# Optimization experiments

Measured on AMD Instinct MI355X. Metric: run time of the kernel, lower is better.

## Reference

```python
import jax, jax.numpy as jnp
import numpy as np

N = 100000      # nodes
E = 500000      # edges
F_IN = 165      # Elliptic feature dim
HID = 128       # hidden
HEADS = 2
DH = HID // HEADS  # 64, per-head GAT out dim
EPS = 1e-5


def setup_inputs() -> dict:
    key = jax.random.key(0)
    ks = jax.random.split(key, 40)

    def w(k, shape, fan_in):
        return (jax.random.normal(k, shape, jnp.float32) / np.sqrt(fan_in)).astype(jnp.float32)

    def bn_params(k, d):
        k1, k2 = jax.random.split(k)
        return (jnp.ones((d,), jnp.float32),                       # gamma
                jnp.zeros((d,), jnp.float32),                      # beta
                0.1 * jax.random.normal(k1, (d,), jnp.float32),    # running mean
                jax.random.uniform(k2, (d,), jnp.float32, 0.5, 1.5))  # running var

    bn1 = bn_params(ks[10], HID)
    bn2 = bn_params(ks[11], HID)
    bn3 = bn_params(ks[12], DH)

    return {
        "x": jax.random.normal(ks[0], (N, F_IN), jnp.float32),
        "edge_index": jax.random.randint(ks[1], (2, E), 0, N, jnp.int32),
        # input_proj
        "w_in": w(ks[2], (F_IN, HID), F_IN), "b_in": jnp.zeros((HID,), jnp.float32),
        # GCNConv
        "w_gcn": w(ks[3], (HID, HID), HID), "b_gcn": jnp.zeros((HID,), jnp.float32),
        "bn1_g": bn1[0], "bn1_b": bn1[1], "bn1_m": bn1[2], "bn1_v": bn1[3],
        # GATConv (heads=2, out=64, concat)
        "w_gat": w(ks[4], (HID, HEADS * DH), HID),
        "att_src": 0.1 * jax.random.normal(ks[5], (HEADS, DH), jnp.float32),
        "att_dst": 0.1 * jax.random.normal(ks[6], (HEADS, DH), jnp.float32),
        "b_gat": jnp.zeros((HEADS * DH,), jnp.float32),
        "bn2_g": bn2[0], "bn2_b": bn2[1], "bn2_m": bn2[2], "bn2_v": bn2[3],
        # SAGEConv (mean aggr)
        "w_sage_l": w(ks[7], (HID, DH), HID), "b_sage": jnp.zeros((DH,), jnp.float32),
        "w_sage_r": w(ks[8], (HID, DH), HID),
        "bn3_g": bn3[0], "bn3_b": bn3[1], "bn3_m": bn3[2], "bn3_v": bn3[3],
        # residual proj + classifier
        "w_res": w(ks[9], (HID, DH), HID), "b_res": jnp.zeros((DH,), jnp.float32),
        "w_c1": w(ks[13], (DH, 32), DH), "b_c1": jnp.zeros((32,), jnp.float32),
        "w_c2": w(ks[14], (32, 2), 32), "b_c2": jnp.zeros((2,), jnp.float32),
    }


def _bn(h, g, b, m, v):
    # eval-mode BatchNorm1d with running stats
    return (h - m) * (g / jnp.sqrt(v + EPS)) + b


def reference(x, edge_index, w_in, b_in, w_gcn, b_gcn,
              bn1_g, bn1_b, bn1_m, bn1_v,
              w_gat, att_src, att_dst, b_gat,
              bn2_g, bn2_b, bn2_m, bn2_v,
              w_sage_l, b_sage, w_sage_r,
              bn3_g, bn3_b, bn3_m, bn3_v,
              w_res, b_res, w_c1, b_c1, w_c2, b_c2):
    n = x.shape[0]
    src, dst = edge_index[0], edge_index[1]
    loop = jnp.arange(n, dtype=src.dtype)
    src_l = jnp.concatenate([src, loop])   # edges + self loops (GCN & GAT)
    dst_l = jnp.concatenate([dst, loop])

    # ---- input_proj (dropout = identity in eval) ----
    h = jax.nn.elu(x @ w_in + b_in)
    residual = h

    hw = h @ w_gcn
    deg = jax.ops.segment_sum(jnp.ones_like(dst_l, jnp.float32), dst_l, n)
    dinv = jnp.where(deg > 0, jax.lax.rsqrt(deg), 0.0)
    norm = dinv[src_l] * dinv[dst_l]                      # [E+N]
    h1 = jax.ops.segment_sum(hw[src_l] * norm[:, None], dst_l, n) + b_gcn
    h1 = jax.nn.elu(_bn(h1, bn1_g, bn1_b, bn1_m, bn1_v))

    # ---- GATConv (heads=2, concat, self loops, leaky_relu 0.2) ----
    g = (h1 @ w_gat).reshape(n, HEADS, DH)
    a_src = jnp.sum(g * att_src, axis=-1)                 # [N, H]
    a_dst = jnp.sum(g * att_dst, axis=-1)
    e = jax.nn.leaky_relu(a_src[src_l] + a_dst[dst_l], 0.2)   # [E+N, H]
    mx = jax.ops.segment_max(e, dst_l, n)                 # per-dst softmax max
    ex = jnp.exp(e - mx[dst_l])
    denom = jax.ops.segment_sum(ex, dst_l, n)
    alpha = ex / (denom[dst_l] + 1e-16)                   # [E+N, H]
    h2 = jax.ops.segment_sum(g[src_l] * alpha[:, :, None], dst_l, n)
    h2 = h2.reshape(n, HEADS * DH) + b_gat
    h2 = jax.nn.elu(_bn(h2, bn2_g, bn2_b, bn2_m, bn2_v))

    # ---- SAGEConv: W_l mean(neighbors) + W_r x + b (no self loops) ----
    deg_s = jax.ops.segment_sum(jnp.ones_like(dst, jnp.float32), dst, n)
    mean_nb = jax.ops.segment_sum(h2[src], dst, n) / jnp.maximum(deg_s, 1.0)[:, None]
    h3 = mean_nb @ w_sage_l + b_sage + h2 @ w_sage_r
    h3 = _bn(h3, bn3_g, bn3_b, bn3_m, bn3_v)
    h3 = jax.nn.elu(h3 + residual @ w_res + b_res)

    # ---- classifier ----
    z = jax.nn.elu(h3 @ w_c1 + b_c1)
    return z @ w_c2 + b_c2
```

## Files before the change

### kernel.cpp

```cpp
#include <hip/hip_runtime.h>
#include <cstdint>
#include <cstddef>

#define BN_EPS 1e-5f

typedef __attribute__((ext_vector_type(8))) short short8v;
typedef __attribute__((ext_vector_type(4))) float float4v;
typedef __attribute__((ext_vector_type(4))) unsigned int uint4v;
typedef unsigned int uint32;
typedef unsigned short ushort16;

__device__ __forceinline__ float elu_f(float v){ return v > 0.f ? v : expm1f(v); }
__device__ __forceinline__ float leaky_f(float v){ return v > 0.f ? v : 0.2f*v; }
__device__ __forceinline__ uint32 f2bf(float f){
  uint32 b = __float_as_uint(f);
  return (b + 0x7fffu + ((b >> 16) & 1u)) >> 16;
}
__device__ __forceinline__ float bflo(uint32 u){ return __uint_as_float(u << 16); }
__device__ __forceinline__ float bfhi(uint32 u){ return __uint_as_float(u & 0xffff0000u); }
__device__ __forceinline__ float readlane_f(float v, int l){
  return __int_as_float(__builtin_amdgcn_readlane(__float_as_int(v), l));
}


__global__ void count_deg_kernel(const int* __restrict__ dst, int E, int* __restrict__ cnt){
  int i = blockIdx.x*blockDim.x + threadIdx.x;
  if(i < E) atomicAdd(&cnt[dst[i]], 1);
}

__global__ __launch_bounds__(1024) void scan_blocks(const int* __restrict__ cnt, int n,
                                                    int* __restrict__ part, int* __restrict__ bsum){
  __shared__ int wsum[16];
  int tid = threadIdx.x, lane = tid & 63, w = tid >> 6;
  int i = blockIdx.x*1024 + tid;
  int v = (i < n) ? cnt[i] : 0;
  int sv = v;
#pragma unroll
  for(int o = 1; o < 64; o <<= 1){
    int u = __shfl_up(sv, o);
    if(lane >= o) sv += u;
  }
  if(lane == 63) wsum[w] = sv;
  __syncthreads();
  int woff = 0;
#pragma unroll
  for(int q = 0; q < 16; q++) woff += (q < w) ? wsum[q] : 0;
  if(i < n) part[i] = woff + sv - v;
  if(tid == 1023) bsum[blockIdx.x] = woff + sv;
}

__global__ __launch_bounds__(1024) void scan_bsum(const int* __restrict__ bsum, int nb,
                                                  int* __restrict__ boff, int* __restrict__ rowptr, int n){
  __shared__ int wsum[16];
  int tid = threadIdx.x, lane = tid & 63, w = tid >> 6;
  int v = (tid < nb) ? bsum[tid] : 0;
  int sv = v;
#pragma unroll
  for(int o = 1; o < 64; o <<= 1){
    int u = __shfl_up(sv, o);
    if(lane >= o) sv += u;
  }
  if(lane == 63) wsum[w] = sv;
  __syncthreads();
  int woff = 0;
#pragma unroll
  for(int q = 0; q < 16; q++) woff += (q < w) ? wsum[q] : 0;
  if(tid < nb) boff[tid] = woff + sv - v;
  if(tid == 1023) rowptr[n] = woff + sv;
}

__global__ void scan_add_dinv(const int* __restrict__ part, const int* __restrict__ boff,
                              const int* __restrict__ cnt, int n,
                              int* __restrict__ rowptr, float* __restrict__ dinv){
  int i = blockIdx.x*blockDim.x + threadIdx.x;
  if(i < n){
    rowptr[i] = part[i] + boff[i >> 10];
    dinv[i] = rsqrtf((float)cnt[i] + 1.0f);
  }
}

__global__ void scatter_kernel(const int* __restrict__ src, const int* __restrict__ dst, int E,
                               const int* __restrict__ rowptr, int* __restrict__ fill,
                               int* __restrict__ col){
  int i = blockIdx.x*blockDim.x + threadIdx.x;
  if(i < E){
    int s = src[i], d = dst[i];
    int p = rowptr[d] + atomicAdd(&fill[d], 1);
    col[p] = s;
  }
}


__global__ __launch_bounds__(256) void cvt_x(const float* __restrict__ x, uint2* __restrict__ xb, int total){
  int idx = blockIdx.x*256 + threadIdx.x;
  if(idx >= total) return;
  int row = idx/48;
  int cp = idx - row*48;
  int c = cp*4;
  const float* xr = x + (size_t)row*165;
  float v0 = (c   < 165) ? xr[c]   : 0.f;
  float v1 = (c+1 < 165) ? xr[c+1] : 0.f;
  float v2 = (c+2 < 165) ? xr[c+2] : 0.f;
  float v3 = (c+3 < 165) ? xr[c+3] : 0.f;
  xb[idx] = make_uint2(f2bf(v0) | (f2bf(v1) << 16), f2bf(v2) | (f2bf(v3) << 16));
}


__global__ void prep_scales(const float* __restrict__ bn1_g, const float* __restrict__ bn1_b,
    const float* __restrict__ bn1_m, const float* __restrict__ bn1_v, const float* __restrict__ b_gcn,
    const float* __restrict__ bn2_g, const float* __restrict__ bn2_b,
    const float* __restrict__ bn2_m, const float* __restrict__ bn2_v, const float* __restrict__ b_gat,
    const float* __restrict__ att_s, const float* __restrict__ att_d,
    const float* __restrict__ bn3_g, const float* __restrict__ bn3_b,
    const float* __restrict__ bn3_m, const float* __restrict__ bn3_v,
    const float* __restrict__ b_sage, const float* __restrict__ b_res,
    float* __restrict__ s1, float* __restrict__ b1c,
    float* __restrict__ s2, float* __restrict__ b2c,
    float* __restrict__ atts2, float* __restrict__ attd2,
    float* __restrict__ s3, float* __restrict__ bias3){
  int c = threadIdx.x;
  float v1 = bn1_g[c]*rsqrtf(bn1_v[c] + BN_EPS);
  s1[c] = v1;
  b1c[c] = (b_gcn[c] - bn1_m[c])*v1 + bn1_b[c];
  float v2 = bn2_g[c]*rsqrtf(bn2_v[c] + BN_EPS);
  s2[c] = v2;
  b2c[c] = (b_gat[c] - bn2_m[c])*v2 + bn2_b[c];
  atts2[c] = att_s[c]/v2;
  attd2[c] = att_d[c]/v2;
  if(c < 64){
    float v3 = bn3_g[c]*rsqrtf(bn3_v[c] + BN_EPS);
    s3[c] = v3;
    bias3[c] = (b_sage[c] - bn3_m[c])*v3 + bn3_b[c] + b_res[c];
  }
}


__device__ __forceinline__ void pack_region(const float* __restrict__ W, int K, int NOUT, int kbase, int idx,
                                            const float* __restrict__ scale, ushort16* __restrict__ out){
  int k = idx / NOUT, c = idx - k*NOUT;
  float v = (k < K) ? W[(size_t)k*NOUT + c] : 0.f;
  if(scale) v *= scale[c];
  int pk = kbase + k;
  out[(size_t)(pk >> 3)*NOUT*8 + (size_t)c*8 + (pk & 7)] = (ushort16)f2bf(v);
}

__global__ __launch_bounds__(256) void pack_all(const float* __restrict__ w_in, const float* __restrict__ w_gcn,
    const float* __restrict__ w_gat, const float* __restrict__ w_sl, const float* __restrict__ w_sr,
    const float* __restrict__ w_res,
    const float* __restrict__ s1, const float* __restrict__ s2, const float* __restrict__ s3,
    ushort16* __restrict__ pw_in, ushort16* __restrict__ pw_gcn,
    ushort16* __restrict__ pw_gat, ushort16* __restrict__ pw_cat){
  int b = blockIdx.x, t = threadIdx.x;
  if(b < 96)       pack_region(w_in,  165, 128, 0,   b*256 + t,        nullptr, pw_in);
  else if(b < 160) pack_region(w_gcn, 128, 128, 0,   (b-96)*256 + t,   s1,      pw_gcn);
  else if(b < 224) pack_region(w_gat, 128, 128, 0,   (b-160)*256 + t,  s2,      pw_gat);
  else if(b < 256) pack_region(w_sl,  128, 64,  0,   (b-224)*256 + t,  s3,      pw_cat);
  else if(b < 288) pack_region(w_sr,  128, 64,  128, (b-256)*256 + t,  s3,      pw_cat);
  else             pack_region(w_res, 128, 64,  256, (b-288)*256 + t,  nullptr, pw_cat);
}


template<int KSTEPS, int NOUT, int EPI>
__global__ __launch_bounds__(256) void mfma_gemm(
    const ushort16* __restrict__ A, int lda,
    const uint4v* __restrict__ pw,
    const float* __restrict__ bias,
    void* __restrict__ out, int ldo, int N,
    const float* __restrict__ dinv,
    const float* __restrict__ atts2, const float* __restrict__ attd2,
    float* __restrict__ a_src, float* __restrict__ a_dst,
    float* __restrict__ ess)
{
  constexpr int SLICE = 4*NOUT;
  constexpr int PT = SLICE/256;
  __shared__ uint4v wlds[2][SLICE];
  int t = threadIdx.x;
  int wid = t >> 6, lane = t & 63;
  int wm, wn;
  if(NOUT == 128){ wm = wid >> 1; wn = wid & 1; } else { wm = wid; wn = 0; }
  constexpr int MTILE = (NOUT == 128) ? 128 : 256;
  long row0 = (long)blockIdx.x*MTILE + wm*64;
  int l15 = lane & 15, lk = lane >> 4;
  int wn64 = wn*64;

  float4v acc[4][4];
#pragma unroll
  for(int fm = 0; fm < 4; fm++)
#pragma unroll
    for(int fn = 0; fn < 4; fn++) acc[fm][fn] = (float4v){0.f,0.f,0.f,0.f};

  const ushort16* abase[4];
#pragma unroll
  for(int fm = 0; fm < 4; fm++){
    long r = row0 + fm*16 + l15;
    if(r > (long)N - 1) r = (long)N - 1;
    abase[fm] = A + r*(size_t)lda + lk*8;
  }

  uint4v rst[PT];
#pragma unroll
  for(int i = 0; i < PT; i++) rst[i] = pw[i*256 + t];
#pragma unroll
  for(int i = 0; i < PT; i++) wlds[0][i*256 + t] = rst[i];
  if(KSTEPS > 1){
#pragma unroll
    for(int i = 0; i < PT; i++) rst[i] = pw[SLICE + i*256 + t];
  }
  short8v a[4];
#pragma unroll
  for(int fm = 0; fm < 4; fm++) a[fm] = *(const short8v*)(abase[fm]);
  __syncthreads();

#pragma unroll
  for(int ks = 0; ks < KSTEPS; ks++){
    short8v b[4];
#pragma unroll
    for(int fn = 0; fn < 4; fn++)
      b[fn] = *(const short8v*)&wlds[ks & 1][lk*NOUT + wn64 + fn*16 + l15];
    short8v an[4];
    if(ks + 1 < KSTEPS){
#pragma unroll
      for(int fm = 0; fm < 4; fm++) an[fm] = *(const short8v*)(abase[fm] + (ks + 1)*32);
    }
#pragma unroll
    for(int fm = 0; fm < 4; fm++)
#pragma unroll
      for(int fn = 0; fn < 4; fn++)
        acc[fm][fn] = __builtin_amdgcn_mfma_f32_16x16x32_bf16(b[fn], a[fm], acc[fm][fn], 0, 0, 0);
    if(ks + 1 < KSTEPS){
#pragma unroll
      for(int i = 0; i < PT; i++) wlds[(ks + 1) & 1][i*256 + t] = rst[i];
      if(ks + 2 < KSTEPS){
#pragma unroll
        for(int i = 0; i < PT; i++) rst[i] = pw[(size_t)(ks + 2)*SLICE + i*256 + t];
      }
#pragma unroll
      for(int fm = 0; fm < 4; fm++) a[fm] = an[fm];
    }
    __syncthreads();
  }

#pragma unroll
  for(int fm = 0; fm < 4; fm++){
    long r = row0 + fm*16 + l15;
    if(r < N){
      float dr = 0.f;
      if constexpr(EPI == 4) dr = dinv[r];
#pragma unroll
      for(int fn = 0; fn < 4; fn++){
        int c0 = wn64 + fn*16 + lk*4;
        float v0 = acc[fm][fn][0], v1 = acc[fm][fn][1];
        float v2 = acc[fm][fn][2], v3 = acc[fm][fn][3];
        if constexpr(EPI == 1){
          float4 bs = *(const float4*)(bias + c0);
          v0 = elu_f(v0 + bs.x); v1 = elu_f(v1 + bs.y);
          v2 = elu_f(v2 + bs.z); v3 = elu_f(v3 + bs.w);
        }
        if constexpr(EPI == 4){ v0 *= dr; v1 *= dr; v2 *= dr; v3 *= dr; }
        uint2 ov = make_uint2(f2bf(v0) | (f2bf(v1) << 16), f2bf(v2) | (f2bf(v3) << 16));
        *(uint2*)((ushort16*)out + r*(size_t)ldo + c0) = ov;
      }
    }
  }

  if constexpr(EPI == 3){
    float4 asv[4], adv[4];
#pragma unroll
    for(int fn = 0; fn < 4; fn++){
      int c0 = wn64 + fn*16 + lk*4;
      asv[fn] = *(const float4*)(atts2 + c0);
      adv[fn] = *(const float4*)(attd2 + c0);
    }
#pragma unroll
    for(int fm = 0; fm < 4; fm++){
      float p1 = 0.f, p2 = 0.f;
#pragma unroll
      for(int fn = 0; fn < 4; fn++){
        p1 += acc[fm][fn][0]*asv[fn].x + acc[fm][fn][1]*asv[fn].y
            + acc[fm][fn][2]*asv[fn].z + acc[fm][fn][3]*asv[fn].w;
        p2 += acc[fm][fn][0]*adv[fn].x + acc[fm][fn][1]*adv[fn].y
            + acc[fm][fn][2]*adv[fn].z + acc[fm][fn][3]*adv[fn].w;
      }
      p1 += __shfl_xor(p1, 16); p1 += __shfl_xor(p1, 32);
      p2 += __shfl_xor(p2, 16); p2 += __shfl_xor(p2, 32);
      long r = row0 + fm*16 + l15;
      if(lane < 16 && r < N){
        a_src[2*r + wn] = p1;
        a_dst[2*r + wn] = p2;
        ess[2*r + wn] = __expf(leaky_f(p1 + p2));
      }
    }
  }
}


__global__ __launch_bounds__(256) void gcn_agg(const uint32* __restrict__ hw2,
    const int* __restrict__ rowptr, const int* __restrict__ col,
    const float* __restrict__ dinv, const float* __restrict__ b1c,
    uint32* __restrict__ h1, int N)
{
  int t = threadIdx.x & 63;
  int w = __builtin_amdgcn_readfirstlane(threadIdx.x >> 6);
  float2 bc = ((const float2*)b1c)[t];
  int stride = gridDim.x*8;
  for(int i0 = (blockIdx.x*4 + w)*2; i0 < N; i0 += stride){
    int i1 = i0 + 1;
    bool has1 = i1 < N;
    int beg0 = rowptr[i0];
    int end0 = rowptr[i0+1];
    int beg1 = end0;
    int end1 = has1 ? rowptr[i1+1] : end0;
    float di0 = dinv[i0];
    float di1 = has1 ? dinv[i1] : 0.f;
    uint32 su0 = hw2[(size_t)i0*64 + t];
    float a00 = bflo(su0), a01 = bfhi(su0);
    float a10 = 0.f, a11 = 0.f;
    if(has1){ uint32 su1 = hw2[(size_t)i1*64 + t]; a10 = bflo(su1); a11 = bfhi(su1); }
#define R0(q) { int row = __builtin_amdgcn_readlane(s0, q); \
    uint32 u = hw2[(size_t)row*64 + t]; a00 += bflo(u); a01 += bfhi(u); }
#define R1(q) { int row = __builtin_amdgcn_readlane(s1, q); \
    uint32 u = hw2[(size_t)row*64 + t]; a10 += bflo(u); a11 += bfhi(u); }
    for(int c0 = beg0, c1 = beg1; c0 < end0 || c1 < end1; c0 += 64, c1 += 64){
      int p0 = c0 + t, p1 = c1 + t;
      int s0 = (p0 < end0) ? col[p0] : 0;
      int s1 = (p1 < end1) ? col[p1] : 0;
      int cl0 = end0 - c0; cl0 = cl0 < 0 ? 0 : (cl0 > 64 ? 64 : cl0);
      int cl1 = end1 - c1; cl1 = cl1 < 0 ? 0 : (cl1 > 64 ? 64 : cl1);
      int m = cl0 < cl1 ? cl0 : cl1;
      int q = 0;
      for(; q + 2 <= m; q += 2){ R0(q) R1(q) R0(q+1) R1(q+1) }
      for(; q < m; q++){ R0(q) R1(q) }
      for(int qa = m; qa < cl0; qa++){ R0(qa) }
      for(int qb = m; qb < cl1; qb++){ R1(qb) }
    }
#undef R0
#undef R1
    h1[(size_t)i0*64 + t] = f2bf(elu_f(a00*di0 + bc.x)) | (f2bf(elu_f(a01*di0 + bc.y)) << 16);
    if(has1)
      h1[(size_t)i1*64 + t] = f2bf(elu_f(a10*di1 + bc.x)) | (f2bf(elu_f(a11*di1 + bc.y)) << 16);
  }
}


__global__ __launch_bounds__(256) void gat_gather(const uint32* __restrict__ g,
    const int* __restrict__ rowptr, const int* __restrict__ col,
    const float* __restrict__ a_src, const float* __restrict__ a_dst,
    const float* __restrict__ ess, const float* __restrict__ b2c,
    uint32* __restrict__ h2out, int N)
{
  int t = threadIdx.x & 63;
  int w = __builtin_amdgcn_readfirstlane(threadIdx.x >> 6);
  float2 bc = ((const float2*)b2c)[t];
  int hl = t >> 5;
  int stride = gridDim.x*4;
  for(int i = blockIdx.x*4 + w; i < N; i += stride){
    int beg = rowptr[i], end = rowptr[i+1];
    int deg = end - beg;
    float2 ad = ((const float2*)a_dst)[i];
    float sw0 = ess[2*i], sw1 = ess[2*i+1];
    float d0 = 0.f, d1 = 0.f, a0 = 0.f, a1 = 0.f;
#define GAT_ROWF(q) { int row = __builtin_amdgcn_readlane(s, q); \
    float w0q = readlane_f(e0, q); \
    float w1q = readlane_f(e1, q); \
    float wq = hl ? w1q : w0q; \
    uint32 u = g[(size_t)row*64 + t]; a0 += wq*bflo(u); a1 += wq*bfhi(u); }
    if(deg <= 64){
      int p = beg + t;
      int s = 0; float e0 = 0.f, e1 = 0.f;
      if(p < end){
        s = col[p];
        float2 as = ((const float2*)a_src)[s];
        e0 = __expf(leaky_f(as.x + ad.x));
        e1 = __expf(leaky_f(as.y + ad.y));
      }
      d0 = e0; d1 = e1;
      int q = 0;
      for(; q + 4 <= deg; q += 4){ GAT_ROWF(q) GAT_ROWF(q+1) GAT_ROWF(q+2) GAT_ROWF(q+3) }
      for(; q < deg; q++){ GAT_ROWF(q) }
    } else {
      for(int c0 = beg; c0 < end; c0 += 64){
        int p = c0 + t;
        int cl = end - c0; if(cl > 64) cl = 64;
        float e0 = 0.f, e1 = 0.f; int s = 0;
        if(p < end){
          s = col[p];
          float2 as = ((const float2*)a_src)[s];
          e0 = __expf(leaky_f(as.x + ad.x));
          e1 = __expf(leaky_f(as.y + ad.y));
        }
        d0 += e0; d1 += e1;
        int q = 0;
        for(; q + 4 <= cl; q += 4){ GAT_ROWF(q) GAT_ROWF(q+1) GAT_ROWF(q+2) GAT_ROWF(q+3) }
        for(; q < cl; q++){ GAT_ROWF(q) }
      }
    }
#undef GAT_ROWF
#pragma unroll
    for(int o = 32; o > 0; o >>= 1){ d0 += __shfl_xor(d0, o); d1 += __shfl_xor(d1, o); }
    float rD = 1.f/(((hl ? d1 : d0) + (hl ? sw1 : sw0)) + 1e-16f);
    float sw = hl ? sw1 : sw0;
    uint32 su = g[(size_t)i*64 + t];
    float v0 = (a0 + sw*bflo(su))*rD + bc.x;
    float v1 = (a1 + sw*bfhi(su))*rD + bc.y;
    h2out[(size_t)i*192 + t] = f2bf(elu_f(v0)) | (f2bf(elu_f(v1)) << 16);
  }
}


__global__ __launch_bounds__(256) void sage_mean(const uint32* __restrict__ h2,
    const int* __restrict__ rowptr, const int* __restrict__ col,
    uint32* __restrict__ mout, int N)
{
  int t = threadIdx.x & 63;
  int w = __builtin_amdgcn_readfirstlane(threadIdx.x >> 6);
  int stride = gridDim.x*8;
  for(int i0 = (blockIdx.x*4 + w)*2; i0 < N; i0 += stride){
    int i1 = i0 + 1;
    bool has1 = i1 < N;
    int beg0 = rowptr[i0];
    int end0 = rowptr[i0+1];
    int beg1 = end0;
    int end1 = has1 ? rowptr[i1+1] : end0;
    float a00 = 0.f, a01 = 0.f, a10 = 0.f, a11 = 0.f;
#define S0(q) { int row = __builtin_amdgcn_readlane(s0, q); \
    uint32 u = h2[(size_t)row*192 + t]; a00 += bflo(u); a01 += bfhi(u); }
#define S1(q) { int row = __builtin_amdgcn_readlane(s1, q); \
    uint32 u = h2[(size_t)row*192 + t]; a10 += bflo(u); a11 += bfhi(u); }
    for(int c0 = beg0, c1 = beg1; c0 < end0 || c1 < end1; c0 += 64, c1 += 64){
      int p0 = c0 + t, p1 = c1 + t;
      int s0 = (p0 < end0) ? col[p0] : 0;
      int s1 = (p1 < end1) ? col[p1] : 0;
      int cl0 = end0 - c0; cl0 = cl0 < 0 ? 0 : (cl0 > 64 ? 64 : cl0);
      int cl1 = end1 - c1; cl1 = cl1 < 0 ? 0 : (cl1 > 64 ? 64 : cl1);
      int m = cl0 < cl1 ? cl0 : cl1;
      int q = 0;
      for(; q + 2 <= m; q += 2){ S0(q) S1(q) S0(q+1) S1(q+1) }
      for(; q < m; q++){ S0(q) S1(q) }
      for(int qa = m; qa < cl0; qa++){ S0(qa) }
      for(int qb = m; qb < cl1; qb++){ S1(qb) }
    }
#undef S0
#undef S1
    float inv0 = 1.f/fmaxf((float)(end0 - beg0), 1.f);
    mout[(size_t)i0*192 + t] = f2bf(a00*inv0) | (f2bf(a01*inv0) << 16);
    if(has1){
      float inv1 = 1.f/fmaxf((float)(end1 - beg1), 1.f);
      mout[(size_t)i1*192 + t] = f2bf(a10*inv1) | (f2bf(a11*inv1) << 16);
    }
  }
}


__global__ __launch_bounds__(256) void classifier_kernel(const uint32* __restrict__ h3,
    const float* __restrict__ w1, const float* __restrict__ b1,
    const float* __restrict__ w2, const float* __restrict__ b2,
    float* __restrict__ out, int N)
{
  __shared__ float hs[8][64];
  __shared__ float zs[8][32];
  int node0 = blockIdx.x*8;
  int t = threadIdx.x;
  {
    int r = t >> 5, cp = t & 31;
    int nd = node0 + r;
    uint32 u = (nd < N) ? h3[(size_t)nd*32 + cp] : 0u;
    hs[r][2*cp]   = bflo(u);
    hs[r][2*cp+1] = bfhi(u);
  }
  __syncthreads();
  int nn = t >> 5, ln = t & 31;
  float acc = b1[ln];
#pragma unroll
  for(int k = 0; k < 64; k++) acc += hs[nn][k]*w1[k*32 + ln];
  zs[nn][ln] = elu_f(acc);
  __syncthreads();
  int node = node0 + nn;
  if(ln < 2 && node < N){
    float o = b2[ln];
#pragma unroll
    for(int k = 0; k < 32; k++) o += zs[nn][k]*w2[k*2 + ln];
    out[(size_t)node*2 + ln] = o;
  }
}


extern "C" void kernel_launch(void* const* d_in, const int* in_sizes, int n_in,
                              void* d_out, int out_size, void* d_ws, size_t ws_size,
                              hipStream_t stream)
{
  (void)n_in; (void)out_size; (void)ws_size;
  const float* x      = (const float*)d_in[0];
  const int*   ei     = (const int*)  d_in[1];
  const float* w_in   = (const float*)d_in[2];
  const float* b_in   = (const float*)d_in[3];
  const float* w_gcn  = (const float*)d_in[4];
  const float* b_gcn  = (const float*)d_in[5];
  const float* bn1_g  = (const float*)d_in[6];
  const float* bn1_b  = (const float*)d_in[7];
  const float* bn1_m  = (const float*)d_in[8];
  const float* bn1_v  = (const float*)d_in[9];
  const float* w_gat  = (const float*)d_in[10];
  const float* att_s  = (const float*)d_in[11];
  const float* att_d  = (const float*)d_in[12];
  const float* b_gat  = (const float*)d_in[13];
  const float* bn2_g  = (const float*)d_in[14];
  const float* bn2_b  = (const float*)d_in[15];
  const float* bn2_m  = (const float*)d_in[16];
  const float* bn2_v  = (const float*)d_in[17];
  const float* w_sl   = (const float*)d_in[18];
  const float* b_sage = (const float*)d_in[19];
  const float* w_sr   = (const float*)d_in[20];
  const float* bn3_g  = (const float*)d_in[21];
  const float* bn3_b  = (const float*)d_in[22];
  const float* bn3_m  = (const float*)d_in[23];
  const float* bn3_v  = (const float*)d_in[24];
  const float* w_res  = (const float*)d_in[25];
  const float* b_res  = (const float*)d_in[26];
  const float* w_c1   = (const float*)d_in[27];
  const float* b_c1   = (const float*)d_in[28];
  const float* w_c2   = (const float*)d_in[29];
  const float* b_c2   = (const float*)d_in[30];

  const int F_IN = 165;
  int N = in_sizes[0]/F_IN;
  int E = in_sizes[1]/2;
  const int* srcp = ei;
  const int* dstp = ei + E;
  int nb = (N + 1023) >> 10;

  char* p = (char*)d_ws;
  auto alloc = [&](size_t bytes) -> char* {
    char* q = p; p += (bytes + 255) & ~(size_t)255; return q;
  };
  ushort16* Acat  = (ushort16*)alloc((size_t)N*384*2);
  ushort16* xb    = (ushort16*)alloc((size_t)N*192*2);
  ushort16* bufG  = (ushort16*)alloc((size_t)N*128*2);
  float* a_src    = (float*)alloc((size_t)N*2*4);
  float* a_dst    = (float*)alloc((size_t)N*2*4);
  float* ess      = (float*)alloc((size_t)N*2*4);
  float* dinv     = (float*)alloc((size_t)N*4);
  int* cnt        = (int*)alloc((size_t)N*4);
  int* fill       = (int*)alloc((size_t)N*4);
  int* rowptr     = (int*)alloc((size_t)(N+1)*4);
  int* part       = (int*)alloc((size_t)N*4);
  int* bsum       = (int*)alloc(1024*4);
  int* boff       = (int*)alloc(1024*4);
  int* col        = (int*)alloc((size_t)E*4);
  float* s1       = (float*)alloc(128*4);
  float* b1c      = (float*)alloc(128*4);
  float* s2       = (float*)alloc(128*4);
  float* b2c      = (float*)alloc(128*4);
  float* atts2    = (float*)alloc(128*4);
  float* attd2    = (float*)alloc(128*4);
  float* s3       = (float*)alloc(64*4);
  float* bias3    = (float*)alloc(64*4);
  ushort16* pw_in  = (ushort16*)alloc(6*4*128*16);
  ushort16* pw_gcn = (ushort16*)alloc(4*4*128*16);
  ushort16* pw_gat = (ushort16*)alloc(4*4*128*16);
  ushort16* pw_cat = (ushort16*)alloc(12*4*64*16);

  ushort16* h1 = xb;
  ushort16* h3 = bufG;

  hipMemsetAsync(cnt, 0, (size_t)((char*)(fill + N) - (char*)cnt), stream);

  count_deg_kernel<<<(E+255)/256, 256, 0, stream>>>(dstp, E, cnt);
  scan_blocks<<<nb, 1024, 0, stream>>>(cnt, N, part, bsum);
  scan_bsum<<<1, 1024, 0, stream>>>(bsum, nb, boff, rowptr, N);
  scan_add_dinv<<<(N+255)/256, 256, 0, stream>>>(part, boff, cnt, N, rowptr, dinv);
  scatter_kernel<<<(E+255)/256, 256, 0, stream>>>(srcp, dstp, E, rowptr, fill, col);

  cvt_x<<<(N*48 + 255)/256, 256, 0, stream>>>(x, (uint2*)xb, N*48);
  prep_scales<<<1, 128, 0, stream>>>(bn1_g, bn1_b, bn1_m, bn1_v, b_gcn,
                                     bn2_g, bn2_b, bn2_m, bn2_v, b_gat,
                                     att_s, att_d,
                                     bn3_g, bn3_b, bn3_m, bn3_v, b_sage, b_res,
                                     s1, b1c, s2, b2c, atts2, attd2, s3, bias3);
  pack_all<<<320, 256, 0, stream>>>(w_in, w_gcn, w_gat, w_sl, w_sr, w_res,
                                    s1, s2, s3, pw_in, pw_gcn, pw_gat, pw_cat);

  int g128 = (N + 127)/128;
  int g256 = (N + 255)/256;
  int gagg = (N + 3)/4; if(gagg > 4096) gagg = 4096;
  int gpair = (N + 7)/8; if(gpair > 4096) gpair = 4096;

  mfma_gemm<6,128,1><<<g128, 256, 0, stream>>>(xb, 192, (const uint4v*)pw_in, b_in,
      (void*)(Acat + 256), 384, N, nullptr, nullptr, nullptr, nullptr, nullptr, nullptr);
  mfma_gemm<4,128,4><<<g128, 256, 0, stream>>>(Acat + 256, 384, (const uint4v*)pw_gcn, nullptr,
      (void*)bufG, 128, N, dinv, nullptr, nullptr, nullptr, nullptr, nullptr);
  gcn_agg<<<gpair, 256, 0, stream>>>((const uint32*)bufG, rowptr, col, dinv, b1c,
                                     (uint32*)h1, N);
  mfma_gemm<4,128,3><<<g128, 256, 0, stream>>>(h1, 128, (const uint4v*)pw_gat, nullptr,
      (void*)bufG, 128, N, nullptr, atts2, attd2, a_src, a_dst, ess);
  gat_gather<<<gagg, 256, 0, stream>>>((const uint32*)bufG, rowptr, col, a_src, a_dst, ess,
                                       b2c, (uint32*)Acat + 64, N);
  sage_mean<<<gpair, 256, 0, stream>>>((const uint32*)Acat + 64, rowptr, col, (uint32*)Acat, N);
  mfma_gemm<12,64,1><<<g256, 256, 0, stream>>>(Acat, 384, (const uint4v*)pw_cat, bias3,
      (void*)h3, 64, N, nullptr, nullptr, nullptr, nullptr, nullptr, nullptr);
  classifier_kernel<<<(N+7)/8, 256, 0, stream>>>((const uint32*)h3, w_c1, b_c1, w_c2, b_c2,
                                                 (float*)d_out, N);
}
```

Measured before the change: 316.8 us.

## Project SAGE features before neighbor mean to gather 64-wide rows

Uses linearity of the mean to apply W_sage_l (with BN scale) to h2 first, producing a 64-dim y per node. The neighbor mean then gathers these 64-wide bf16 rows instead of 128-wide h2 rows, halving gather bytes. The final GEMM only covers h2·W_r and residual·W_res, and adds the gathered mean in a new epilogue. The cost is an extra small GEMM launch, plus extra buffers and a second rounding of the projected values to bf16 before the mean.

```diff
diff --git a/kernel.cpp b/kernel.cpp
--- a/kernel.cpp
+++ b/kernel.cpp
@@ -149,14 +149,14 @@
     const float* __restrict__ w_res,
     const float* __restrict__ s1, const float* __restrict__ s2, const float* __restrict__ s3,
     ushort16* __restrict__ pw_in, ushort16* __restrict__ pw_gcn,
-    ushort16* __restrict__ pw_gat, ushort16* __restrict__ pw_cat){
+    ushort16* __restrict__ pw_gat, ushort16* __restrict__ pw_sl, ushort16* __restrict__ pw_cat2){
   int b = blockIdx.x, t = threadIdx.x;
   if(b < 96)       pack_region(w_in,  165, 128, 0,   b*256 + t,        nullptr, pw_in);
   else if(b < 160) pack_region(w_gcn, 128, 128, 0,   (b-96)*256 + t,   s1,      pw_gcn);
   else if(b < 224) pack_region(w_gat, 128, 128, 0,   (b-160)*256 + t,  s2,      pw_gat);
-  else if(b < 256) pack_region(w_sl,  128, 64,  0,   (b-224)*256 + t,  s3,      pw_cat);
-  else if(b < 288) pack_region(w_sr,  128, 64,  128, (b-256)*256 + t,  s3,      pw_cat);
-  else             pack_region(w_res, 128, 64,  256, (b-288)*256 + t,  nullptr, pw_cat);
+  else if(b < 256) pack_region(w_sl,  128, 64,  0,   (b-224)*256 + t,  s3,      pw_sl);
+  else if(b < 288) pack_region(w_sr,  128, 64,  0,   (b-256)*256 + t,  s3,      pw_cat2);
+  else             pack_region(w_res, 128, 64,  128, (b-288)*256 + t,  nullptr, pw_cat2);
 }
 
 
@@ -169,7 +169,7 @@
     const float* __restrict__ dinv,
     const float* __restrict__ atts2, const float* __restrict__ attd2,
     float* __restrict__ a_src, float* __restrict__ a_dst,
-    float* __restrict__ ess)
+    float* __restrict__ ess, const uint32* __restrict__ mny)
 {
   constexpr int SLICE = 4*NOUT;
   constexpr int PT = SLICE/256;
@@ -257,6 +257,14 @@
           v2 = elu_f(v2 + bs.z); v3 = elu_f(v3 + bs.w);
         }
         if constexpr(EPI == 4){ v0 *= dr; v1 *= dr; v2 *= dr; v3 *= dr; }
+        if constexpr(EPI == 5){
+          uint2 m2 = *(const uint2*)(mny + r*(size_t)32 + (c0 >> 1));
+          float4 bs = *(const float4*)(bias + c0);
+          v0 = elu_f(v0 + bflo(m2.x) + bs.x);
+          v1 = elu_f(v1 + bfhi(m2.x) + bs.y);
+          v2 = elu_f(v2 + bflo(m2.y) + bs.z);
+          v3 = elu_f(v3 + bfhi(m2.y) + bs.w);
+        }
         uint2 ov = make_uint2(f2bf(v0) | (f2bf(v1) << 16), f2bf(v2) | (f2bf(v3) << 16));
         *(uint2*)((ushort16*)out + r*(size_t)ldo + c0) = ov;
       }
@@ -402,50 +410,39 @@
     uint32 su = g[(size_t)i*64 + t];
     float v0 = (a0 + sw*bflo(su))*rD + bc.x;
     float v1 = (a1 + sw*bfhi(su))*rD + bc.y;
-    h2out[(size_t)i*192 + t] = f2bf(elu_f(v0)) | (f2bf(elu_f(v1)) << 16);
-  }
-}
-
-
-__global__ __launch_bounds__(256) void sage_mean(const uint32* __restrict__ h2,
+    h2out[(size_t)i*128 + t] = f2bf(elu_f(v0)) | (f2bf(elu_f(v1)) << 16);
+  }
+}
+
+
+__global__ __launch_bounds__(256) void sage_mean_y(const uint32* __restrict__ y,
     const int* __restrict__ rowptr, const int* __restrict__ col,
     uint32* __restrict__ mout, int N)
 {
   int t = threadIdx.x & 63;
   int w = __builtin_amdgcn_readfirstlane(threadIdx.x >> 6);
-  int stride = gridDim.x*8;
-  for(int i0 = (blockIdx.x*4 + w)*2; i0 < N; i0 += stride){
-    int i1 = i0 + 1;
-    bool has1 = i1 < N;
-    int beg0 = rowptr[i0];
-    int end0 = rowptr[i0+1];
-    int beg1 = end0;
-    int end1 = has1 ? rowptr[i1+1] : end0;
-    float a00 = 0.f, a01 = 0.f, a10 = 0.f, a11 = 0.f;
-#define S0(q) { int row = __builtin_amdgcn_readlane(s0, q); \
-    uint32 u = h2[(size_t)row*192 + t]; a00 += bflo(u); a01 += bfhi(u); }
-#define S1(q) { int row = __builtin_amdgcn_readlane(s1, q); \
-    uint32 u = h2[(size_t)row*192 + t]; a10 += bflo(u); a11 += bfhi(u); }
-    for(int c0 = beg0, c1 = beg1; c0 < end0 || c1 < end1; c0 += 64, c1 += 64){
-      int p0 = c0 + t, p1 = c1 + t;
-      int s0 = (p0 < end0) ? col[p0] : 0;
-      int s1 = (p1 < end1) ? col[p1] : 0;
-      int cl0 = end0 - c0; cl0 = cl0 < 0 ? 0 : (cl0 > 64 ? 64 : cl0);
-      int cl1 = end1 - c1; cl1 = cl1 < 0 ? 0 : (cl1 > 64 ? 64 : cl1);
-      int m = cl0 < cl1 ? cl0 : cl1;
-      int q = 0;
-      for(; q + 2 <= m; q += 2){ S0(q) S1(q) S0(q+1) S1(q+1) }
-      for(; q < m; q++){ S0(q) S1(q) }
-      for(int qa = m; qa < cl0; qa++){ S0(qa) }
-      for(int qb = m; qb < cl1; qb++){ S1(qb) }
-    }
-#undef S0
-#undef S1
-    float inv0 = 1.f/fmaxf((float)(end0 - beg0), 1.f);
-    mout[(size_t)i0*192 + t] = f2bf(a00*inv0) | (f2bf(a01*inv0) << 16);
-    if(has1){
-      float inv1 = 1.f/fmaxf((float)(end1 - beg1), 1.f);
-      mout[(size_t)i1*192 + t] = f2bf(a10*inv1) | (f2bf(a11*inv1) << 16);
+  int hl = t >> 5, l31 = t & 31;
+  int stride = gridDim.x*4;
+  for(int i = blockIdx.x*4 + w; i < N; i += stride){
+    int beg = rowptr[i], end = rowptr[i+1];
+    float a0 = 0.f, a1 = 0.f;
+    for(int c0 = beg; c0 < end; c0 += 64){
+      int p = c0 + t;
+      int cl = end - c0; if(cl > 64) cl = 64;
+      int s = (p < end) ? col[p] : 0;
+      for(int q = 0; q < cl; q += 2){
+        int idx = q + hl;
+        bool valid = idx < cl;
+        int row = __shfl(s, valid ? idx : q);
+        uint32 u = y[(size_t)row*32 + l31];
+        if(valid){ a0 += bflo(u); a1 += bfhi(u); }
+      }
+    }
+    a0 += __shfl_xor(a0, 32);
+    a1 += __shfl_xor(a1, 32);
+    if(hl == 0){
+      float inv = 1.f/fmaxf((float)(end - beg), 1.f);
+      mout[(size_t)i*32 + l31] = f2bf(a0*inv) | (f2bf(a1*inv) << 16);
     }
   }
 }
@@ -532,9 +529,11 @@
   auto alloc = [&](size_t bytes) -> char* {
     char* q = p; p += (bytes + 255) & ~(size_t)255; return q;
   };
-  ushort16* Acat  = (ushort16*)alloc((size_t)N*384*2);
+  ushort16* Acat  = (ushort16*)alloc((size_t)N*256*2);
   ushort16* xb    = (ushort16*)alloc((size_t)N*192*2);
   ushort16* bufG  = (ushort16*)alloc((size_t)N*128*2);
+  ushort16* ybuf  = (ushort16*)alloc((size_t)N*64*2);
+  ushort16* mny   = (ushort16*)alloc((size_t)N*64*2);
   float* a_src    = (float*)alloc((size_t)N*2*4);
   float* a_dst    = (float*)alloc((size_t)N*2*4);
   float* ess      = (float*)alloc((size_t)N*2*4);
@@ -554,10 +553,11 @@
   float* attd2    = (float*)alloc(128*4);
   float* s3       = (float*)alloc(64*4);
   float* bias3    = (float*)alloc(64*4);
-  ushort16* pw_in  = (ushort16*)alloc(6*4*128*16);
-  ushort16* pw_gcn = (ushort16*)alloc(4*4*128*16);
-  ushort16* pw_gat = (ushort16*)alloc(4*4*128*16);
-  ushort16* pw_cat = (ushort16*)alloc(12*4*64*16);
+  ushort16* pw_in   = (ushort16*)alloc(6*4*128*16);
+  ushort16* pw_gcn  = (ushort16*)alloc(4*4*128*16);
+  ushort16* pw_gat  = (ushort16*)alloc(4*4*128*16);
+  ushort16* pw_sl   = (ushort16*)alloc(4*4*64*16);
+  ushort16* pw_cat2 = (ushort16*)alloc(8*4*64*16);
 
   ushort16* h1 = xb;
   ushort16* h3 = bufG;
@@ -577,7 +577,7 @@
                                      bn3_g, bn3_b, bn3_m, bn3_v, b_sage, b_res,
                                      s1, b1c, s2, b2c, atts2, attd2, s3, bias3);
   pack_all<<<320, 256, 0, stream>>>(w_in, w_gcn, w_gat, w_sl, w_sr, w_res,
-                                    s1, s2, s3, pw_in, pw_gcn, pw_gat, pw_cat);
+                                    s1, s2, s3, pw_in, pw_gcn, pw_gat, pw_sl, pw_cat2);
 
   int g128 = (N + 127)/128;
   int g256 = (N + 255)/256;
@@ -585,18 +585,20 @@
   int gpair = (N + 7)/8; if(gpair > 4096) gpair = 4096;
 
   mfma_gemm<6,128,1><<<g128, 256, 0, stream>>>(xb, 192, (const uint4v*)pw_in, b_in,
-      (void*)(Acat + 256), 384, N, nullptr, nullptr, nullptr, nullptr, nullptr, nullptr);
-  mfma_gemm<4,128,4><<<g128, 256, 0, stream>>>(Acat + 256, 384, (const uint4v*)pw_gcn, nullptr,
-      (void*)bufG, 128, N, dinv, nullptr, nullptr, nullptr, nullptr, nullptr);
+      (void*)(Acat + 128), 256, N, nullptr, nullptr, nullptr, nullptr, nullptr, nullptr, nullptr);
+  mfma_gemm<4,128,4><<<g128, 256, 0, stream>>>(Acat + 128, 256, (const uint4v*)pw_gcn, nullptr,
+      (void*)bufG, 128, N, dinv, nullptr, nullptr, nullptr, nullptr, nullptr, nullptr);
   gcn_agg<<<gpair, 256, 0, stream>>>((const uint32*)bufG, rowptr, col, dinv, b1c,
                                      (uint32*)h1, N);
   mfma_gemm<4,128,3><<<g128, 256, 0, stream>>>(h1, 128, (const uint4v*)pw_gat, nullptr,
-      (void*)bufG, 128, N, nullptr, atts2, attd2, a_src, a_dst, ess);
+      (void*)bufG, 128, N, nullptr, atts2, attd2, a_src, a_dst, ess, nullptr);
   gat_gather<<<gagg, 256, 0, stream>>>((const uint32*)bufG, rowptr, col, a_src, a_dst, ess,
-                                       b2c, (uint32*)Acat + 64, N);
-  sage_mean<<<gpair, 256, 0, stream>>>((const uint32*)Acat + 64, rowptr, col, (uint32*)Acat, N);
-  mfma_gemm<12,64,1><<<g256, 256, 0, stream>>>(Acat, 384, (const uint4v*)pw_cat, bias3,
-      (void*)h3, 64, N, nullptr, nullptr, nullptr, nullptr, nullptr, nullptr);
+                                       b2c, (uint32*)Acat, N);
+  mfma_gemm<4,64,0><<<g256, 256, 0, stream>>>(Acat, 256, (const uint4v*)pw_sl, nullptr,
+      (void*)ybuf, 64, N, nullptr, nullptr, nullptr, nullptr, nullptr, nullptr, nullptr);
+  sage_mean_y<<<gagg, 256, 0, stream>>>((const uint32*)ybuf, rowptr, col, (uint32*)mny, N);
+  mfma_gemm<8,64,5><<<g256, 256, 0, stream>>>(Acat, 256, (const uint4v*)pw_cat2, bias3,
+      (void*)h3, 64, N, nullptr, nullptr, nullptr, nullptr, nullptr, nullptr, (const uint32*)mny);
   classifier_kernel<<<(N+7)/8, 256, 0, stream>>>((const uint32*)h3, w_c1, b_c1, w_c2, b_c2,
                                                  (float*)d_out, N);
 }
```

After: 325.1 us. +2.6%, slower.
